# Kernel tuning notes

Measured on AMD Instinct MI355X. Metric: run time of the kernel, lower is better.

The kernel has to match this reference:

```python
import jax, jax.numpy as jnp
import numpy as np

N = 100000      # nodes
E = 3200000     # edges (avg degree 32)
F_IN = 512
HID = 256
CLS = 64


def _linear_init(k, fan_in, fan_out):
    lim = 1.0 / np.sqrt(fan_in)
    kw, kb = jax.random.split(k)
    W = jax.random.uniform(kw, (fan_in, fan_out), jnp.float32, -lim, lim)
    b = jax.random.uniform(kb, (fan_out,), jnp.float32, -lim, lim)
    return W, b


def setup_inputs() -> dict:
    key = jax.random.key(0)
    ks = jax.random.split(key, 8)
    x = jax.random.normal(ks[0], (N, F_IN), jnp.float32)
    edge_src = jax.random.randint(ks[1], (E,), 0, N, jnp.int32)
    off = jax.random.randint(ks[2], (E,), 1, N, jnp.int32)
    edge_dst = ((edge_src + off) % N).astype(jnp.int32)  # no self loops
    Wm0, bm0 = _linear_init(ks[3], F_IN, HID)
    Wv0, bv0 = _linear_init(ks[4], F_IN, HID)
    Wm1, bm1 = _linear_init(ks[5], HID, CLS)
    Wv1, bv1 = _linear_init(ks[6], HID, CLS)
    sample = jax.random.normal(ks[7], (N, CLS), jnp.float32)
    return dict(x=x, Wm0=Wm0, bm0=bm0, Wv0=Wv0, bv0=bv0,
                Wm1=Wm1, bm1=bm1, Wv1=Wv1, bv1=bv1,
                sample=sample, edge_src=edge_src, edge_dst=edge_dst)


def reference(x, Wm0, bm0, Wv0, bv0, Wm1, bm1, Wv1, bv1, sample, edge_src, edge_dst):
    n = x.shape[0]
    loops = jnp.arange(n, dtype=edge_src.dtype)
    src = jnp.concatenate([edge_src, loops])  # fill_diag(adj, 1.0)
    dst = jnp.concatenate([edge_dst, loops])
    ones = jnp.ones(src.shape[0], x.dtype)
    deg = jax.ops.segment_sum(ones, src, num_segments=n)
    dis = jnp.where(deg > 0, deg ** -0.5, 0.0)   # D^-0.5
    di = jnp.where(deg > 0, 1.0 / deg, 0.0)      # D^-1
    w0 = dis[src] * dis[dst]                      # adj0 = D^-0.5 A D^-0.5
    w1 = di[src] * di[dst]                        # adj1 = D^-1  A D^-1

    def spmm(w, m):  # (adj @ m) with edge weights w
        return jax.ops.segment_sum(w[:, None] * m[dst], src, num_segments=n)

    # layer 0 (initial=True): no aggregation, dropout off (eval)
    mean = jax.nn.elu(x @ Wm0 + bm0)
    var = jax.nn.relu(x @ Wv0 + bv0)
    # layer 1: variance-attention + dual SpMM
    mean = jax.nn.elu(mean @ Wm1 + bm1)
    var = jax.nn.relu(var @ Wv1 + bv1) + 1e-6
    attn = jnp.exp(-var)
    mean = spmm(w0, mean * attn)
    var = spmm(w1, var * attn * attn)

    out = mean + sample * jnp.sqrt(var)
    return jax.nn.log_softmax(out, axis=-1)
```

## Files before the change

kernel.cpp:

```cpp
#include <hip/hip_runtime.h>
#include <cstdint>
#include <cstddef>


typedef _Float16 h8 __attribute__((ext_vector_type(8)));
typedef _Float16 h2 __attribute__((ext_vector_type(2)));
typedef float f32x4 __attribute__((ext_vector_type(4)));
typedef unsigned int uint32;

#define BSHIFT 7
#define NCHUNK 256

static __device__ __forceinline__ float elu_f(float z) {
  return z > 0.f ? z : expm1f(z);
}

__global__ __launch_bounds__(256) void hist_k(const int* __restrict__ esrc, int E,
                                              int chunk, int* __restrict__ h, int NB) {
  __shared__ int sh[1024];
  int t = threadIdx.x;
  for (int i = t; i < NB; i += 256) sh[i] = 0;
  __syncthreads();
  int e0 = blockIdx.x * chunk;
  int e1 = min(e0 + chunk, E);
  for (int e = e0 + t; e < e1; e += 256) atomicAdd(&sh[esrc[e] >> BSHIFT], 1);
  __syncthreads();
  for (int i = t; i < NB; i += 256) h[blockIdx.x * NB + i] = sh[i];
}

__global__ __launch_bounds__(256) void btotal_k(const int* __restrict__ h,
                                                int* __restrict__ tot, int NB) {
  int b = blockIdx.x, t = threadIdx.x;
  int v = h[t * NB + b];
#pragma unroll
  for (int off = 32; off; off >>= 1) v += __shfl_xor(v, off, 64);
  __shared__ int sw[4];
  if ((t & 63) == 0) sw[t >> 6] = v;
  __syncthreads();
  if (t == 0) tot[b] = sw[0] + sw[1] + sw[2] + sw[3];
}

__global__ __launch_bounds__(1024) void bscan_k(const int* __restrict__ tot,
                                                int* __restrict__ base, int NB) {
  __shared__ int sh[1024];
  int t = threadIdx.x;
  int v = (t < NB) ? tot[t] : 0;
  sh[t] = v;
  __syncthreads();
  for (int off = 1; off < 1024; off <<= 1) {
    int add = (t >= off) ? sh[t - off] : 0;
    __syncthreads();
    sh[t] += add;
    __syncthreads();
  }
  if (t < NB) base[t] = sh[t] - v;
  if (t == 1023) base[NB] = sh[1023];
}

__global__ __launch_bounds__(256) void boff_k(int* __restrict__ h,
                                              const int* __restrict__ base, int NB) {
  __shared__ int sh[256];
  int b = blockIdx.x, t = threadIdx.x;
  int v = h[t * NB + b];
  sh[t] = v;
  __syncthreads();
  for (int off = 1; off < 256; off <<= 1) {
    int add = (t >= off) ? sh[t - off] : 0;
    __syncthreads();
    sh[t] += add;
    __syncthreads();
  }
  h[t * NB + b] = base[b] + sh[t] - v;
}

__global__ __launch_bounds__(256) void bscatter_k(
    const int* __restrict__ esrc, const int* __restrict__ edst, int E, int chunk,
    const int* __restrict__ h, int* __restrict__ psrc, int* __restrict__ pdst, int NB) {
  __shared__ int lcur[1024];
  int t = threadIdx.x;
  for (int i = t; i < NB; i += 256) lcur[i] = h[blockIdx.x * NB + i];
  __syncthreads();
  int e0 = blockIdx.x * chunk;
  int e1 = min(e0 + chunk, E);
  for (int e = e0 + t; e < e1; e += 256) {
    int s = esrc[e], d = edst[e];
    int pos = atomicAdd(&lcur[s >> BSHIFT], 1);
    psrc[pos] = s;
    pdst[pos] = d;
  }
}

__global__ __launch_bounds__(256) void countN_k(
    const int* __restrict__ psrc, const int* __restrict__ base,
    int* __restrict__ cnt, int n) {
  __shared__ int c128[128];
  int b = blockIdx.x, t = threadIdx.x;
  if (t < 128) c128[t] = 0;
  __syncthreads();
  int lo = base[b], hi = base[b + 1];
  for (int i = lo + t; i < hi; i += 256) atomicAdd(&c128[psrc[i] & 127], 1);
  __syncthreads();
  if (t < 128) {
    int node = b * 128 + t;
    if (node < n) cnt[node] = c128[t];
  }
}

__global__ __launch_bounds__(256) void partC_k(
    const int* __restrict__ psrc, const int* __restrict__ pdst,
    const int* __restrict__ base, const int* __restrict__ rs,
    int* __restrict__ csr, int n) {
  __shared__ int lcur[128];
  int b = blockIdx.x, t = threadIdx.x;
  if (t < 128) {
    int node = b * 128 + t;
    lcur[t] = (node < n) ? rs[node] : 0;
  }
  __syncthreads();
  int lo = base[b], hi = base[b + 1];
  for (int i = lo + t; i < hi; i += 256) {
    int pos = atomicAdd(&lcur[psrc[i] & 127], 1);
    csr[pos] = pdst[i];
  }
}

__global__ void deg_fin_k(const int* __restrict__ cnt, float2* __restrict__ dd, int n) {
  int v = blockIdx.x * 256 + threadIdx.x;
  if (v < n) {
    float d = (float)(cnt[v] + 1);
    dd[v] = make_float2(rsqrtf(d), 1.f / d);
  }
}

__global__ void scan1_k(const int* __restrict__ cnt, int* __restrict__ excl,
                        int* __restrict__ bsum, int n) {
  __shared__ int sh[256];
  int t = threadIdx.x, idx = blockIdx.x * 256 + t;
  int v = (idx < n) ? ((cnt[idx] + 3) & ~3) : 0;
  sh[t] = v;
  __syncthreads();
  for (int off = 1; off < 256; off <<= 1) {
    int add = (t >= off) ? sh[t - off] : 0;
    __syncthreads();
    sh[t] += add;
    __syncthreads();
  }
  if (idx < n) excl[idx] = sh[t] - v;
  if (t == 255) bsum[blockIdx.x] = sh[255];
}

__global__ void scan2_k(const int* __restrict__ bsum, int* __restrict__ boff, int nb) {
  __shared__ int sh[512];
  int t = threadIdx.x;
  int v = (t < nb) ? bsum[t] : 0;
  sh[t] = v;
  __syncthreads();
  for (int off = 1; off < 512; off <<= 1) {
    int add = (t >= off) ? sh[t - off] : 0;
    __syncthreads();
    sh[t] += add;
    __syncthreads();
  }
  if (t < nb) boff[t] = sh[t] - v;
}

__global__ void scan3_k(int* __restrict__ excl, const int* __restrict__ boff, int n) {
  int idx = blockIdx.x * 256 + threadIdx.x;
  if (idx < n) excl[idx] += boff[blockIdx.x];
}

__global__ void prep_w_k(const float* __restrict__ Wm0, const float* __restrict__ Wv0,
                         const float* __restrict__ Wm1, const float* __restrict__ Wv1,
                         _Float16* __restrict__ W1t, _Float16* __restrict__ W2t) {
  int idx = blockIdx.x * 256 + threadIdx.x;
  if (idx < 512 * 512) {
    int n = idx >> 9, k = idx & 511;
    float v = (n < 256) ? Wm0[k * 256 + n] : Wv0[k * 256 + (n - 256)];
    W1t[idx] = (_Float16)v;
  }
  if (idx < 128 * 512) {
    int n = idx >> 9, k = idx & 511;
    float v = 0.f;
    if (n < 64) { if (k < 256) v = Wm1[k * 64 + n]; }
    else        { if (k >= 256) v = Wv1[(k - 256) * 64 + (n - 64)]; }
    W2t[idx] = (_Float16)v;
  }
}

__global__ __launch_bounds__(256) void gemm1_k(
    const float* __restrict__ A, const _Float16* __restrict__ Bt,
    const float* __restrict__ b0, const float* __restrict__ b1,
    _Float16* __restrict__ out, int M, int K) {
  __shared__ _Float16 As[128 * 40];
  __shared__ _Float16 Bs[128 * 40];
  const int bid = blockIdx.x;
  const int mt = bid >> 2, nt = bid & 3;
  const int m0 = mt * 128, n0 = nt * 128;
  const int t = threadIdx.x;
  const int lane = t & 63;
  const int wave = t >> 6;
  const int wm = wave >> 1, wn = wave & 1;
  const int lr = lane & 15, quad = lane >> 4;

  f32x4 acc[4][4] = {};

  for (int kt = 0; kt < K; kt += 32) {
#pragma unroll
    for (int i = 0; i < 2; i++) {
      int c = t + i * 256;
      int row = c >> 2, kc = (c & 3) * 8;
      int gr = m0 + row;
      if (gr > M - 1) gr = M - 1;
      const float* srcf = A + (size_t)gr * K + kt + kc;
      float4 f0 = ((const float4*)srcf)[0];
      float4 f1 = ((const float4*)srcf)[1];
      *(h8*)&As[row * 40 + kc] =
          h8{(_Float16)f0.x, (_Float16)f0.y, (_Float16)f0.z, (_Float16)f0.w,
             (_Float16)f1.x, (_Float16)f1.y, (_Float16)f1.z, (_Float16)f1.w};
      *(h8*)&Bs[row * 40 + kc] =
          *(const h8*)(Bt + (size_t)(n0 + row) * K + kt + kc);
    }
    __syncthreads();
    h8 af[4], bf[4];
#pragma unroll
    for (int i = 0; i < 4; i++)
      af[i] = *(h8*)&As[(wm * 64 + i * 16 + lr) * 40 + quad * 8];
#pragma unroll
    for (int j = 0; j < 4; j++)
      bf[j] = *(h8*)&Bs[(wn * 64 + j * 16 + lr) * 40 + quad * 8];
#pragma unroll
    for (int i = 0; i < 4; i++)
#pragma unroll
      for (int j = 0; j < 4; j++)
        acc[i][j] = __builtin_amdgcn_mfma_f32_16x16x32_f16(af[i], bf[j], acc[i][j], 0, 0, 0);
    __syncthreads();
  }

#pragma unroll
  for (int j = 0; j < 4; j++) {
    int gc = n0 + wn * 64 + j * 16 + lr;
    float bj = (gc < 256) ? b0[gc] : b1[gc - 256];
#pragma unroll
    for (int i = 0; i < 4; i++) {
#pragma unroll
      for (int r = 0; r < 4; r++) {
        int gr = m0 + wm * 64 + i * 16 + quad * 4 + r;
        if (gr < M) {
          float z = acc[i][j][r] + bj;
          float v = (gc < 256) ? elu_f(z) : fmaxf(z, 0.f);
          out[(size_t)gr * 512 + gc] = (_Float16)v;
        }
      }
    }
  }
}

__global__ __launch_bounds__(256) void gemm2_k(
    const _Float16* __restrict__ A, const _Float16* __restrict__ Bt,
    const float* __restrict__ bm1, const float* __restrict__ bv1,
    uint32* __restrict__ Mcat, int M, int K) {
  __shared__ _Float16 As[128 * 40];
  __shared__ _Float16 Bs[128 * 40];
  const int m0 = blockIdx.x * 128;
  const int t = threadIdx.x;
  const int lane = t & 63;
  const int wave = t >> 6;
  const int lr = lane & 15, quad = lane >> 4;

  f32x4 acc[2][8] = {};

  for (int kt = 0; kt < K; kt += 32) {
#pragma unroll
    for (int i = 0; i < 2; i++) {
      int c = t + i * 256;
      int row = c >> 2, kc = (c & 3) * 8;
      int gr = m0 + row;
      if (gr > M - 1) gr = M - 1;
      *(h8*)&As[row * 40 + kc] = *(const h8*)(A + (size_t)gr * K + kt + kc);
      *(h8*)&Bs[row * 40 + kc] = *(const h8*)(Bt + (size_t)row * K + kt + kc);
    }
    __syncthreads();
    h8 af[2], bf[8];
#pragma unroll
    for (int i = 0; i < 2; i++)
      af[i] = *(h8*)&As[(wave * 32 + i * 16 + lr) * 40 + quad * 8];
#pragma unroll
    for (int j = 0; j < 8; j++)
      bf[j] = *(h8*)&Bs[(j * 16 + lr) * 40 + quad * 8];
#pragma unroll
    for (int i = 0; i < 2; i++)
#pragma unroll
      for (int j = 0; j < 8; j++)
        acc[i][j] = __builtin_amdgcn_mfma_f32_16x16x32_f16(af[i], bf[j], acc[i][j], 0, 0, 0);
    __syncthreads();
  }

#pragma unroll
  for (int jm = 0; jm < 4; jm++) {
    int c = jm * 16 + lr;
    float bm = bm1[c], bv = bv1[c];
#pragma unroll
    for (int i = 0; i < 2; i++) {
#pragma unroll
      for (int r = 0; r < 4; r++) {
        int gr = m0 + wave * 32 + i * 16 + quad * 4 + r;
        if (gr < M) {
          float zm = acc[i][jm][r] + bm;
          float zv = acc[i][4 + jm][r] + bv;
          float m = elu_f(zm);
          float v = fmaxf(zv, 0.f) + 1e-6f;
          float a = __expf(-v);
          h2 pk;
          pk.x = (_Float16)(m * a);
          pk.y = (_Float16)(v * a * a);
          Mcat[(size_t)gr * 64 + c] = __builtin_bit_cast(uint32, pk);
        }
      }
    }
  }
}

__global__ __launch_bounds__(256) void spmm_final_k(
    const uint32* __restrict__ Mcat, const float2* __restrict__ dd,
    const int* __restrict__ row_start, const int* __restrict__ cnt,
    const int* __restrict__ csr, const float* __restrict__ sample,
    float* __restrict__ out, int n) {
  int wid = threadIdx.x >> 6, lane = threadIdx.x & 63;
  int r = blockIdx.x * 4 + wid;
  if (r >= n) return;
  float2 wr = dd[r];
  h2 self = __builtin_bit_cast(h2, Mcat[(size_t)r * 64 + lane]);
  float Sm = wr.x * (float)self.x;
  float Sv = wr.y * (float)self.y;
  int start = __builtin_amdgcn_readfirstlane(row_start[r]);
  int c = __builtin_amdgcn_readfirstlane(cnt[r]);
  int j = 0;
  for (; j + 4 <= c; j += 4) {
    int4 d4 = *(const int4*)(csr + start + j);
    float2 w0 = dd[d4.x];
    float2 w1 = dd[d4.y];
    float2 w2 = dd[d4.z];
    float2 w3 = dd[d4.w];
    h2 p0 = __builtin_bit_cast(h2, Mcat[(size_t)d4.x * 64 + lane]);
    h2 p1 = __builtin_bit_cast(h2, Mcat[(size_t)d4.y * 64 + lane]);
    h2 p2 = __builtin_bit_cast(h2, Mcat[(size_t)d4.z * 64 + lane]);
    h2 p3 = __builtin_bit_cast(h2, Mcat[(size_t)d4.w * 64 + lane]);
    Sm += w0.x * (float)p0.x; Sv += w0.y * (float)p0.y;
    Sm += w1.x * (float)p1.x; Sv += w1.y * (float)p1.y;
    Sm += w2.x * (float)p2.x; Sv += w2.y * (float)p2.y;
    Sm += w3.x * (float)p3.x; Sv += w3.y * (float)p3.y;
  }
  for (; j < c; j++) {
    int d = csr[start + j];
    float2 w = dd[d];
    h2 p = __builtin_bit_cast(h2, Mcat[(size_t)d * 64 + lane]);
    Sm += w.x * (float)p.x;
    Sv += w.y * (float)p.y;
  }
  float mean = wr.x * Sm;
  float var = wr.y * Sv;
  float o = mean + sample[(size_t)r * 64 + lane] * sqrtf(var);
  float mx = o;
#pragma unroll
  for (int off = 32; off; off >>= 1) mx = fmaxf(mx, __shfl_xor(mx, off, 64));
  float ex = __expf(o - mx);
  float s = ex;
#pragma unroll
  for (int off = 32; off; off >>= 1) s += __shfl_xor(s, off, 64);
  out[(size_t)r * 64 + lane] = o - mx - logf(s);
}

extern "C" void kernel_launch(void* const* d_in, const int* in_sizes, int n_in,
                              void* d_out, int out_size, void* d_ws, size_t ws_size,
                              hipStream_t stream) {
  (void)n_in; (void)out_size; (void)ws_size;
  const float* x    = (const float*)d_in[0];
  const float* Wm0  = (const float*)d_in[1];
  const float* bm0  = (const float*)d_in[2];
  const float* Wv0  = (const float*)d_in[3];
  const float* bv0  = (const float*)d_in[4];
  const float* Wm1  = (const float*)d_in[5];
  const float* bm1  = (const float*)d_in[6];
  const float* Wv1  = (const float*)d_in[7];
  const float* bv1  = (const float*)d_in[8];
  const float* sample = (const float*)d_in[9];
  const int* esrc   = (const int*)d_in[10];
  const int* edst   = (const int*)d_in[11];
  float* out = (float*)d_out;

  const int N = in_sizes[0] / 512;
  const int E = in_sizes[10];
  const int NB = (N + 127) >> BSHIFT;
  const int chunk = (E + NCHUNK - 1) / NCHUNK;

  uint8_t* p = (uint8_t*)d_ws;
  size_t off = 0;
  auto alloc = [&](size_t bytes) -> void* {
    void* r = p + off;
    off += (bytes + 255) & ~(size_t)255;
    return r;
  };
  _Float16* W1t  = (_Float16*)alloc((size_t)512 * 512 * 2);
  _Float16* W2t  = (_Float16*)alloc((size_t)128 * 512 * 2);
  _Float16* Hcat = (_Float16*)alloc((size_t)N * 512 * 2);
  uint32*   Mcat = (uint32*)alloc((size_t)N * 64 * 4);
  int*   cnt    = (int*)alloc((size_t)N * 4);
  float2* dd    = (float2*)alloc((size_t)N * 8);
  int*   rs     = (int*)alloc((size_t)N * 4);
  int*   h      = (int*)alloc((size_t)NCHUNK * NB * 4);
  int*   tot    = (int*)alloc((size_t)(NB + 1) * 4);
  int*   base   = (int*)alloc((size_t)(NB + 1) * 4);
  int*   bsum   = (int*)alloc(2048);
  int*   boff   = (int*)alloc(2048);
  int*   csr    = (int*)alloc((size_t)(E + 4 * N) * 4);
  int* psrc = (int*)Hcat;
  int* pdst = psrc + E;

  const int nbN = (N + 255) / 256;

  prep_w_k<<<(512 * 512 + 255) / 256, 256, 0, stream>>>(Wm0, Wv0, Wm1, Wv1, W1t, W2t);
  hist_k<<<NCHUNK, 256, 0, stream>>>(esrc, E, chunk, h, NB);
  btotal_k<<<NB, 256, 0, stream>>>(h, tot, NB);
  bscan_k<<<1, 1024, 0, stream>>>(tot, base, NB);
  boff_k<<<NB, 256, 0, stream>>>(h, base, NB);
  bscatter_k<<<NCHUNK, 256, 0, stream>>>(esrc, edst, E, chunk, h, psrc, pdst, NB);
  countN_k<<<NB, 256, 0, stream>>>(psrc, base, cnt, N);
  deg_fin_k<<<nbN, 256, 0, stream>>>(cnt, dd, N);
  scan1_k<<<nbN, 256, 0, stream>>>(cnt, rs, bsum, N);
  scan2_k<<<1, 512, 0, stream>>>(bsum, boff, nbN);
  scan3_k<<<nbN, 256, 0, stream>>>(rs, boff, N);
  partC_k<<<NB, 256, 0, stream>>>(psrc, pdst, base, rs, csr, N);

  const int mtiles = (N + 127) / 128;
  gemm1_k<<<mtiles * 4, 256, 0, stream>>>(x, W1t, bm0, bv0, Hcat, N, 512);
  gemm2_k<<<mtiles, 256, 0, stream>>>(Hcat, W2t, bm1, bv1, Mcat, N, 512);
  spmm_final_k<<<(N + 3) / 4, 256, 0, stream>>>(Mcat, dd, rs, cnt, csr, sample, out, N);
}
```

Before: 832.6 us.

## Double-buffer GEMM tiles, swizzle gemm1 blocks, pack edge pairs, fuse degree kernel

Both GEMM kernels now prefetch the next K-slice into registers and write it to a second LDS buffer while the MFMAs run on the current one, so each step needs one barrier instead of two. gemm1 also remaps block IDs so the four N-tiles of a group of eight M-tiles run close together, which is meant to improve L2 reuse of the fp32 x rows. Its epilogue is staged through LDS to produce coalesced 128-bit row stores. On the graph side, src/dst are stored as interleaved int2 pairs and the degree finalisation is folded into countN_k, removing one launch. The cost is more registers and LDS per block, plus an extra sync in the epilogue.

Result: faster. 762.5 us (-8.4%).

```diff
diff --git a/kernel.cpp b/kernel.cpp
--- a/kernel.cpp
+++ b/kernel.cpp
@@ -75,7 +75,7 @@
 
 __global__ __launch_bounds__(256) void bscatter_k(
     const int* __restrict__ esrc, const int* __restrict__ edst, int E, int chunk,
-    const int* __restrict__ h, int* __restrict__ psrc, int* __restrict__ pdst, int NB) {
+    const int* __restrict__ h, int2* __restrict__ pairs, int NB) {
   __shared__ int lcur[1024];
   int t = threadIdx.x;
   for (int i = t; i < NB; i += 256) lcur[i] = h[blockIdx.x * NB + i];
@@ -85,31 +85,34 @@
   for (int e = e0 + t; e < e1; e += 256) {
     int s = esrc[e], d = edst[e];
     int pos = atomicAdd(&lcur[s >> BSHIFT], 1);
-    psrc[pos] = s;
-    pdst[pos] = d;
+    pairs[pos] = make_int2(s, d);
   }
 }
 
 __global__ __launch_bounds__(256) void countN_k(
-    const int* __restrict__ psrc, const int* __restrict__ base,
-    int* __restrict__ cnt, int n) {
+    const int2* __restrict__ pairs, const int* __restrict__ base,
+    int* __restrict__ cnt, float2* __restrict__ dd, int n) {
   __shared__ int c128[128];
   int b = blockIdx.x, t = threadIdx.x;
   if (t < 128) c128[t] = 0;
   __syncthreads();
   int lo = base[b], hi = base[b + 1];
-  for (int i = lo + t; i < hi; i += 256) atomicAdd(&c128[psrc[i] & 127], 1);
+  for (int i = lo + t; i < hi; i += 256) atomicAdd(&c128[pairs[i].x & 127], 1);
   __syncthreads();
   if (t < 128) {
     int node = b * 128 + t;
-    if (node < n) cnt[node] = c128[t];
+    if (node < n) {
+      int c = c128[t];
+      cnt[node] = c;
+      float d = (float)(c + 1);
+      dd[node] = make_float2(rsqrtf(d), 1.f / d);
+    }
   }
 }
 
 __global__ __launch_bounds__(256) void partC_k(
-    const int* __restrict__ psrc, const int* __restrict__ pdst,
-    const int* __restrict__ base, const int* __restrict__ rs,
-    int* __restrict__ csr, int n) {
+    const int2* __restrict__ pairs, const int* __restrict__ base,
+    const int* __restrict__ rs, int* __restrict__ csr, int n) {
   __shared__ int lcur[128];
   int b = blockIdx.x, t = threadIdx.x;
   if (t < 128) {
@@ -119,16 +122,9 @@
   __syncthreads();
   int lo = base[b], hi = base[b + 1];
   for (int i = lo + t; i < hi; i += 256) {
-    int pos = atomicAdd(&lcur[psrc[i] & 127], 1);
-    csr[pos] = pdst[i];
-  }
-}
-
-__global__ void deg_fin_k(const int* __restrict__ cnt, float2* __restrict__ dd, int n) {
-  int v = blockIdx.x * 256 + threadIdx.x;
-  if (v < n) {
-    float d = (float)(cnt[v] + 1);
-    dd[v] = make_float2(rsqrtf(d), 1.f / d);
+    int2 pr = pairs[i];
+    int pos = atomicAdd(&lcur[pr.x & 127], 1);
+    csr[pos] = pr.y;
   }
 }
 
@@ -190,52 +186,92 @@
 __global__ __launch_bounds__(256) void gemm1_k(
     const float* __restrict__ A, const _Float16* __restrict__ Bt,
     const float* __restrict__ b0, const float* __restrict__ b1,
-    _Float16* __restrict__ out, int M, int K) {
-  __shared__ _Float16 As[128 * 40];
-  __shared__ _Float16 Bs[128 * 40];
-  const int bid = blockIdx.x;
-  const int mt = bid >> 2, nt = bid & 3;
+    _Float16* __restrict__ out, int M, int K, int mtiles) {
+  __shared__ _Float16 lds[20480];
+  _Float16* As = lds;
+  _Float16* Bs = lds + 10240;
+
+  const int sg = blockIdx.x >> 5, loc = blockIdx.x & 31;
+  const int nt = loc >> 3, mtl = loc & 7;
+  const int mt = sg * 8 + mtl;
+  if (mt >= mtiles) return;
   const int m0 = mt * 128, n0 = nt * 128;
   const int t = threadIdx.x;
   const int lane = t & 63;
   const int wave = t >> 6;
   const int wm = wave >> 1, wn = wave & 1;
   const int lr = lane & 15, quad = lane >> 4;
+  const int trow = t >> 2;
+  const int tkc = (t & 3) * 8;
+
+  const size_t arow0 = (size_t)min(m0 + trow, M - 1) * K;
+  const size_t arow1 = (size_t)min(m0 + trow + 64, M - 1) * K;
+  const size_t brow0 = (size_t)(n0 + trow) * K;
+  const size_t brow1 = (size_t)(n0 + trow + 64) * K;
 
   f32x4 acc[4][4] = {};
+  float4 pa[2][2];
+  h8 pb[2];
+
+  {
+    const float* s0 = A + arow0 + tkc;
+    const float* s1 = A + arow1 + tkc;
+    pa[0][0] = ((const float4*)s0)[0]; pa[0][1] = ((const float4*)s0)[1];
+    pa[1][0] = ((const float4*)s1)[0]; pa[1][1] = ((const float4*)s1)[1];
+    pb[0] = *(const h8*)(Bt + brow0 + tkc);
+    pb[1] = *(const h8*)(Bt + brow1 + tkc);
+  }
+  {
+    *(h8*)&As[trow * 40 + tkc] =
+        h8{(_Float16)pa[0][0].x, (_Float16)pa[0][0].y, (_Float16)pa[0][0].z, (_Float16)pa[0][0].w,
+           (_Float16)pa[0][1].x, (_Float16)pa[0][1].y, (_Float16)pa[0][1].z, (_Float16)pa[0][1].w};
+    *(h8*)&As[(trow + 64) * 40 + tkc] =
+        h8{(_Float16)pa[1][0].x, (_Float16)pa[1][0].y, (_Float16)pa[1][0].z, (_Float16)pa[1][0].w,
+           (_Float16)pa[1][1].x, (_Float16)pa[1][1].y, (_Float16)pa[1][1].z, (_Float16)pa[1][1].w};
+    *(h8*)&Bs[trow * 40 + tkc] = pb[0];
+    *(h8*)&Bs[(trow + 64) * 40 + tkc] = pb[1];
+  }
+  __syncthreads();
 
   for (int kt = 0; kt < K; kt += 32) {
-#pragma unroll
-    for (int i = 0; i < 2; i++) {
-      int c = t + i * 256;
-      int row = c >> 2, kc = (c & 3) * 8;
-      int gr = m0 + row;
-      if (gr > M - 1) gr = M - 1;
-      const float* srcf = A + (size_t)gr * K + kt + kc;
-      float4 f0 = ((const float4*)srcf)[0];
-      float4 f1 = ((const float4*)srcf)[1];
-      *(h8*)&As[row * 40 + kc] =
-          h8{(_Float16)f0.x, (_Float16)f0.y, (_Float16)f0.z, (_Float16)f0.w,
-             (_Float16)f1.x, (_Float16)f1.y, (_Float16)f1.z, (_Float16)f1.w};
-      *(h8*)&Bs[row * 40 + kc] =
-          *(const h8*)(Bt + (size_t)(n0 + row) * K + kt + kc);
-    }
-    __syncthreads();
+    const int cur = (kt >> 5) & 1;
+    const int curo = cur * 5120;
+    const bool more = (kt + 32) < K;
+    if (more) {
+      const float* s0 = A + arow0 + kt + 32 + tkc;
+      const float* s1 = A + arow1 + kt + 32 + tkc;
+      pa[0][0] = ((const float4*)s0)[0]; pa[0][1] = ((const float4*)s0)[1];
+      pa[1][0] = ((const float4*)s1)[0]; pa[1][1] = ((const float4*)s1)[1];
+      pb[0] = *(const h8*)(Bt + brow0 + kt + 32 + tkc);
+      pb[1] = *(const h8*)(Bt + brow1 + kt + 32 + tkc);
+    }
     h8 af[4], bf[4];
 #pragma unroll
     for (int i = 0; i < 4; i++)
-      af[i] = *(h8*)&As[(wm * 64 + i * 16 + lr) * 40 + quad * 8];
+      af[i] = *(h8*)&As[curo + (wm * 64 + i * 16 + lr) * 40 + quad * 8];
 #pragma unroll
     for (int j = 0; j < 4; j++)
-      bf[j] = *(h8*)&Bs[(wn * 64 + j * 16 + lr) * 40 + quad * 8];
+      bf[j] = *(h8*)&Bs[curo + (wn * 64 + j * 16 + lr) * 40 + quad * 8];
 #pragma unroll
     for (int i = 0; i < 4; i++)
 #pragma unroll
       for (int j = 0; j < 4; j++)
         acc[i][j] = __builtin_amdgcn_mfma_f32_16x16x32_f16(af[i], bf[j], acc[i][j], 0, 0, 0);
-    __syncthreads();
-  }
-
+    if (more) {
+      const int nxto = (cur ^ 1) * 5120;
+      *(h8*)&As[nxto + trow * 40 + tkc] =
+          h8{(_Float16)pa[0][0].x, (_Float16)pa[0][0].y, (_Float16)pa[0][0].z, (_Float16)pa[0][0].w,
+             (_Float16)pa[0][1].x, (_Float16)pa[0][1].y, (_Float16)pa[0][1].z, (_Float16)pa[0][1].w};
+      *(h8*)&As[nxto + (trow + 64) * 40 + tkc] =
+          h8{(_Float16)pa[1][0].x, (_Float16)pa[1][0].y, (_Float16)pa[1][0].z, (_Float16)pa[1][0].w,
+             (_Float16)pa[1][1].x, (_Float16)pa[1][1].y, (_Float16)pa[1][1].z, (_Float16)pa[1][1].w};
+      *(h8*)&Bs[nxto + trow * 40 + tkc] = pb[0];
+      *(h8*)&Bs[nxto + (trow + 64) * 40 + tkc] = pb[1];
+      __syncthreads();
+    }
+  }
+
+  __syncthreads();
 #pragma unroll
   for (int j = 0; j < 4; j++) {
     int gc = n0 + wn * 64 + j * 16 + lr;
@@ -244,13 +280,21 @@
     for (int i = 0; i < 4; i++) {
 #pragma unroll
       for (int r = 0; r < 4; r++) {
-        int gr = m0 + wm * 64 + i * 16 + quad * 4 + r;
-        if (gr < M) {
-          float z = acc[i][j][r] + bj;
-          float v = (gc < 256) ? elu_f(z) : fmaxf(z, 0.f);
-          out[(size_t)gr * 512 + gc] = (_Float16)v;
-        }
+        float z = acc[i][j][r] + bj;
+        float v = (gc < 256) ? elu_f(z) : fmaxf(z, 0.f);
+        lds[(wm * 64 + i * 16 + quad * 4 + r) * 136 + wn * 64 + j * 16 + lr] = (_Float16)v;
       }
+    }
+  }
+  __syncthreads();
+  {
+    const int row = t >> 1, col0 = (t & 1) * 64;
+    const int gr = m0 + row;
+    if (gr < M) {
+      _Float16* dst = out + (size_t)gr * 512 + n0 + col0;
+#pragma unroll
+      for (int k = 0; k < 8; k++)
+        *(h8*)(dst + k * 8) = *(h8*)&lds[row * 136 + col0 + k * 8];
     }
   }
 }
@@ -259,40 +303,65 @@
     const _Float16* __restrict__ A, const _Float16* __restrict__ Bt,
     const float* __restrict__ bm1, const float* __restrict__ bv1,
     uint32* __restrict__ Mcat, int M, int K) {
-  __shared__ _Float16 As[128 * 40];
-  __shared__ _Float16 Bs[128 * 40];
+  __shared__ _Float16 lds[20480];
+  _Float16* As = lds;
+  _Float16* Bs = lds + 10240;
   const int m0 = blockIdx.x * 128;
   const int t = threadIdx.x;
   const int lane = t & 63;
   const int wave = t >> 6;
   const int lr = lane & 15, quad = lane >> 4;
+  const int trow = t >> 2;
+  const int tkc = (t & 3) * 8;
+
+  const size_t arow0 = (size_t)min(m0 + trow, M - 1) * K;
+  const size_t arow1 = (size_t)min(m0 + trow + 64, M - 1) * K;
+  const size_t brow0 = (size_t)trow * K;
+  const size_t brow1 = (size_t)(trow + 64) * K;
 
   f32x4 acc[2][8] = {};
+  h8 pa[2], pb[2];
+
+  pa[0] = *(const h8*)(A + arow0 + tkc);
+  pa[1] = *(const h8*)(A + arow1 + tkc);
+  pb[0] = *(const h8*)(Bt + brow0 + tkc);
+  pb[1] = *(const h8*)(Bt + brow1 + tkc);
+  *(h8*)&As[trow * 40 + tkc] = pa[0];
+  *(h8*)&As[(trow + 64) * 40 + tkc] = pa[1];
+  *(h8*)&Bs[trow * 40 + tkc] = pb[0];
+  *(h8*)&Bs[(trow + 64) * 40 + tkc] = pb[1];
+  __syncthreads();
 
   for (int kt = 0; kt < K; kt += 32) {
-#pragma unroll
-    for (int i = 0; i < 2; i++) {
-      int c = t + i * 256;
-      int row = c >> 2, kc = (c & 3) * 8;
-      int gr = m0 + row;
-      if (gr > M - 1) gr = M - 1;
-      *(h8*)&As[row * 40 + kc] = *(const h8*)(A + (size_t)gr * K + kt + kc);
-      *(h8*)&Bs[row * 40 + kc] = *(const h8*)(Bt + (size_t)row * K + kt + kc);
-    }
-    __syncthreads();
+    const int cur = (kt >> 5) & 1;
+    const int curo = cur * 5120;
+    const bool more = (kt + 32) < K;
+    if (more) {
+      pa[0] = *(const h8*)(A + arow0 + kt + 32 + tkc);
+      pa[1] = *(const h8*)(A + arow1 + kt + 32 + tkc);
+      pb[0] = *(const h8*)(Bt + brow0 + kt + 32 + tkc);
+      pb[1] = *(const h8*)(Bt + brow1 + kt + 32 + tkc);
+    }
     h8 af[2], bf[8];
 #pragma unroll
     for (int i = 0; i < 2; i++)
-      af[i] = *(h8*)&As[(wave * 32 + i * 16 + lr) * 40 + quad * 8];
+      af[i] = *(h8*)&As[curo + (wave * 32 + i * 16 + lr) * 40 + quad * 8];
 #pragma unroll
     for (int j = 0; j < 8; j++)
-      bf[j] = *(h8*)&Bs[(j * 16 + lr) * 40 + quad * 8];
+      bf[j] = *(h8*)&Bs[curo + (j * 16 + lr) * 40 + quad * 8];
 #pragma unroll
     for (int i = 0; i < 2; i++)
 #pragma unroll
       for (int j = 0; j < 8; j++)
         acc[i][j] = __builtin_amdgcn_mfma_f32_16x16x32_f16(af[i], bf[j], acc[i][j], 0, 0, 0);
-    __syncthreads();
+    if (more) {
+      const int nxto = (cur ^ 1) * 5120;
+      *(h8*)&As[nxto + trow * 40 + tkc] = pa[0];
+      *(h8*)&As[nxto + (trow + 64) * 40 + tkc] = pa[1];
+      *(h8*)&Bs[nxto + trow * 40 + tkc] = pb[0];
+      *(h8*)&Bs[nxto + (trow + 64) * 40 + tkc] = pb[1];
+      __syncthreads();
+    }
   }
 
 #pragma unroll
@@ -413,8 +482,7 @@
   int*   bsum   = (int*)alloc(2048);
   int*   boff   = (int*)alloc(2048);
   int*   csr    = (int*)alloc((size_t)(E + 4 * N) * 4);
-  int* psrc = (int*)Hcat;
-  int* pdst = psrc + E;
+  int2* pairs = (int2*)Hcat;
 
   const int nbN = (N + 255) / 256;
 
@@ -423,16 +491,16 @@
   btotal_k<<<NB, 256, 0, stream>>>(h, tot, NB);
   bscan_k<<<1, 1024, 0, stream>>>(tot, base, NB);
   boff_k<<<NB, 256, 0, stream>>>(h, base, NB);
-  bscatter_k<<<NCHUNK, 256, 0, stream>>>(esrc, edst, E, chunk, h, psrc, pdst, NB);
-  countN_k<<<NB, 256, 0, stream>>>(psrc, base, cnt, N);
-  deg_fin_k<<<nbN, 256, 0, stream>>>(cnt, dd, N);
+  bscatter_k<<<NCHUNK, 256, 0, stream>>>(esrc, edst, E, chunk, h, pairs, NB);
+  countN_k<<<NB, 256, 0, stream>>>(pairs, base, cnt, dd, N);
   scan1_k<<<nbN, 256, 0, stream>>>(cnt, rs, bsum, N);
   scan2_k<<<1, 512, 0, stream>>>(bsum, boff, nbN);
   scan3_k<<<nbN, 256, 0, stream>>>(rs, boff, N);
-  partC_k<<<NB, 256, 0, stream>>>(psrc, pdst, base, rs, csr, N);
+  partC_k<<<NB, 256, 0, stream>>>(pairs, base, rs, csr, N);
 
   const int mtiles = (N + 127) / 128;
-  gemm1_k<<<mtiles * 4, 256, 0, stream>>>(x, W1t, bm0, bv0, Hcat, N, 512);
+  const int sgroups = (mtiles + 7) / 8;
+  gemm1_k<<<sgroups * 32, 256, 0, stream>>>(x, W1t, bm0, bv0, Hcat, N, 512, mtiles);
   gemm2_k<<<mtiles, 256, 0, stream>>>(Hcat, W2t, bm1, bv1, Mcat, N, 512);
   spmm_final_k<<<(N + 3) / 4, 256, 0, stream>>>(Mcat, dd, rs, cnt, csr, sample, out, N);
 }
```
